# Kernel optimization log

Measured on AMD Instinct MI355X. Metric: run time of the kernel, lower is better.

Reference implementation:

```python
import jax, jax.numpy as jnp
import numpy as np

BS, C, C2, H, W = 8, 256, 128, 64, 64

def setup_inputs() -> dict:
    key = jax.random.key(0)
    ks = jax.random.split(key, 9)
    s = 0.05
    return {
        "appearance_1": jax.random.normal(ks[0], (BS, C2, H, W), jnp.float32),
        "appearance_2": jax.random.normal(ks[1], (BS, C2, H, W), jnp.float32),
        "motion": jax.random.normal(ks[2], (BS, C, H, W), jnp.float32),
        "Wq": jax.random.normal(ks[3], (C2, C2), jnp.float32) * s,
        "bq": jax.random.normal(ks[4], (C2,), jnp.float32) * s,
        "Wk": jax.random.normal(ks[5], (C2, C2), jnp.float32) * s,
        "bk": jax.random.normal(ks[6], (C2,), jnp.float32) * s,
        "Wv": jax.random.normal(ks[7], (C, C), jnp.float32) * s,
        "bv": jax.random.normal(ks[8], (C,), jnp.float32) * s,
    }

def reference(appearance_1, appearance_2, motion, Wq, bq, Wk, bk, Wv, bv):
    bs, c, h, w = motion.shape
    n = h * w
    a1 = appearance_1.reshape(bs, -1, n)   # [b, C2, N]
    a2 = appearance_2.reshape(bs, -1, n)   # [b, C2, N]
    m = motion.reshape(bs, c, n)           # [b, C,  N]
    # 1x1 convs == per-pixel linear projections
    q = jnp.einsum('oc,bcn->bon', Wq, a2) + bq[None, :, None]  # [b, C2, N]
    k = jnp.einsum('oc,bcn->bon', Wk, a1) + bk[None, :, None]  # [b, C2, N]
    v = jnp.einsum('oc,bcn->bon', Wv, m) + bv[None, :, None]   # [b, C,  N]
    # energy[b, i, j] = <q[:, i], k[:, j]> ; softmax over j
    energy = jnp.einsum('bci,bcj->bij', q, k)                  # [b, N, N]
    attention = jax.nn.softmax(energy, axis=-1)
    # out = V @ attention^T
    out = jnp.einsum('bcj,bij->bci', v, attention)             # [b, C, N]
    out = out.reshape(bs, c, h, w)
    fuse_out = out * motion
    return (fuse_out, out)
```

## Files before the change

kernel.cpp:

```cpp
#include <hip/hip_runtime.h>
#include <cstdint>
#include <cstddef>

#define BS   8
#define C    256
#define C2   128
#define NPIX 4096

typedef unsigned short u16;
typedef unsigned int   u32;
typedef __bf16 bf16_t;
typedef bf16_t bf16x8 __attribute__((ext_vector_type(8)));
typedef float  f32x16 __attribute__((ext_vector_type(16)));

__device__ __forceinline__ u16 f2bf(float f) {
    union { float ff; u32 i; } x; x.ff = f;
    u32 r = x.i + 0x7fffu + ((x.i >> 16) & 1u);
    return (u16)(r >> 16);
}

__device__ __forceinline__ void split2(float f, u16& hi, u16& lo) {
    union { float ff; u32 i; } x; x.ff = f;
    hi = (u16)(x.i >> 16);
    union { u32 i; float ff; } h; h.i = x.i & 0xffff0000u;
    union { float ff; u32 i; } r; r.ff = f - h.ff;
    lo = (u16)(r.i >> 16);
}

__device__ __forceinline__ u32 pk2(u16 a, u16 b) { return (u32)a | ((u32)b << 16); }

__global__ __launch_bounds__(256)
void prep_w(const float* __restrict__ Wq, const float* __restrict__ Wk,
            const float* __restrict__ Wv,
            u16* __restrict__ qh, u16* __restrict__ ql,
            u16* __restrict__ kh, u16* __restrict__ kl,
            u16* __restrict__ vh, u16* __restrict__ vl) {
    const int z = blockIdx.y;
    const int nelem = (z == 2) ? (C * C) : (C2 * C2);
    const int idx = (blockIdx.x * 256 + threadIdx.x) * 4;
    if (idx >= nelem) return;
    const float* src = (z == 0) ? Wq : (z == 1) ? Wk : Wv;
    u16* oh = (z == 0) ? qh : (z == 1) ? kh : vh;
    u16* ol = (z == 0) ? ql : (z == 1) ? kl : vl;
    const float4 v = *(const float4*)(src + idx);
    u16 h[4], l[4];
    split2(v.x, h[0], l[0]); split2(v.y, h[1], l[1]);
    split2(v.z, h[2], l[2]); split2(v.w, h[3], l[3]);
    *(uint2*)(oh + idx) = make_uint2(pk2(h[0], h[1]), pk2(h[2], h[3]));
    *(uint2*)(ol + idx) = make_uint2(pk2(l[0], l[1]), pk2(l[2], l[3]));
}

__global__ __launch_bounds__(256, 4)
void proj_qk(const u16* __restrict__ wh, const u16* __restrict__ wl,
             const float* __restrict__ bias,
             const float* __restrict__ x,
             u16* __restrict__ out) {
    __shared__ __align__(16) u16 Xb[2][2][2][64][8];
    const int t  = threadIdx.x;
    const int w  = t >> 6;
    const int li = t & 31;
    const int hs = (t >> 5) & 1;
    const int n0 = blockIdx.x * 64;
    const int b  = blockIdx.y;

    const int sn = t & 63;
    const int c4 = t >> 6;
    const int sh = c4 >> 1, e0 = (c4 & 1) * 4;

    const float* xbase = x + (size_t)b * C2 * NPIX + n0 + sn;

    f32x16 acc[2];
    #pragma unroll
    for (int nt = 0; nt < 2; ++nt)
        #pragma unroll
        for (int e = 0; e < 16; ++e) acc[nt][e] = 0.f;

    {
        const float* xp = xbase + (size_t)(c4 * 4) * NPIX;
        const float f0 = xp[0], f1 = xp[NPIX], f2 = xp[2 * NPIX], f3 = xp[3 * NPIX];
        u16 h[4], lo[4];
        split2(f0, h[0], lo[0]); split2(f1, h[1], lo[1]);
        split2(f2, h[2], lo[2]); split2(f3, h[3], lo[3]);
        *(uint2*)&Xb[0][0][sh][sn][e0] = make_uint2(pk2(h[0], h[1]), pk2(h[2], h[3]));
        *(uint2*)&Xb[0][1][sh][sn][e0] = make_uint2(pk2(lo[0], lo[1]), pk2(lo[2], lo[3]));
    }
    __syncthreads();

    const size_t wrow = (size_t)(w * 32 + li) * C2;
    for (int ks = 0; ks < 8; ++ks) {
        const int db = ks & 1;
        if (ks < 7) {
            const float* xp = xbase + (size_t)((ks + 1) * 16 + c4 * 4) * NPIX;
            const float f0 = xp[0], f1 = xp[NPIX], f2 = xp[2 * NPIX], f3 = xp[3 * NPIX];
            u16 h[4], lo[4];
            split2(f0, h[0], lo[0]); split2(f1, h[1], lo[1]);
            split2(f2, h[2], lo[2]); split2(f3, h[3], lo[3]);
            *(uint2*)&Xb[db ^ 1][0][sh][sn][e0] = make_uint2(pk2(h[0], h[1]), pk2(h[2], h[3]));
            *(uint2*)&Xb[db ^ 1][1][sh][sn][e0] = make_uint2(pk2(lo[0], lo[1]), pk2(lo[2], lo[3]));
        }
        const int ko = ks * 16 + hs * 8;
        const bf16x8 ah = *(const bf16x8*)(wh + wrow + ko);
        const bf16x8 al = *(const bf16x8*)(wl + wrow + ko);
        #pragma unroll
        for (int nt = 0; nt < 2; ++nt) {
            const bf16x8 bh = *(const bf16x8*)&Xb[db][0][hs][nt * 32 + li][0];
            const bf16x8 bl = *(const bf16x8*)&Xb[db][1][hs][nt * 32 + li][0];
            acc[nt] = __builtin_amdgcn_mfma_f32_32x32x16_bf16(ah, bh, acc[nt], 0, 0, 0);
            acc[nt] = __builtin_amdgcn_mfma_f32_32x32x16_bf16(ah, bl, acc[nt], 0, 0, 0);
            acc[nt] = __builtin_amdgcn_mfma_f32_32x32x16_bf16(al, bh, acc[nt], 0, 0, 0);
        }
        __syncthreads();
    }

    #pragma unroll
    for (int nt = 0; nt < 2; ++nt) {
        const int n = n0 + nt * 32 + li;
        u16* op = out + ((size_t)b * NPIX + n) * C2 + w * 32;
        #pragma unroll
        for (int g = 0; g < 4; ++g) {
            const int ob = 8 * g + 4 * hs;
            u16 p[4];
            #pragma unroll
            for (int j = 0; j < 4; ++j)
                p[j] = f2bf(acc[nt][g * 4 + j] + bias[w * 32 + ob + j]);
            *(uint2*)(op + ob) = make_uint2(pk2(p[0], p[1]), pk2(p[2], p[3]));
        }
    }
}

__global__ __launch_bounds__(256, 2)
void proj_v(const u16* __restrict__ wh, const u16* __restrict__ wl,
            const float* __restrict__ bias,
            const float* __restrict__ x,
            u16* __restrict__ out) {
    __shared__ __align__(16) u16 Xs[2][2][2][128][8];
    __shared__ __align__(16) u16 Ws[2][2][2][128][8];
    const int t  = threadIdx.x;
    const int w  = t >> 6;
    const int li = t & 31;
    const int hs = (t >> 5) & 1;
    const int n0 = blockIdx.x * 128;
    const int o0 = blockIdx.y * 128;
    const int b  = blockIdx.z;

    const int sn = t & 127;
    const int sc = t >> 7;
    const int so = t >> 1;
    const int sh2 = t & 1;

    const float* xbase = x + (size_t)b * C * NPIX + n0 + sn;
    const u16* whb = wh + (size_t)(o0 + so) * C + sh2 * 8;
    const u16* wlb = wl + (size_t)(o0 + so) * C + sh2 * 8;

    f32x16 acc[4];
    #pragma unroll
    for (int ot = 0; ot < 4; ++ot)
        #pragma unroll
        for (int e = 0; e < 16; ++e) acc[ot][e] = 0.f;

    {
        const float* xp = xbase + (size_t)(sc * 8) * NPIX;
        u16 h[8], lo[8];
        #pragma unroll
        for (int j = 0; j < 8; ++j) split2(xp[(size_t)j * NPIX], h[j], lo[j]);
        *(uint4*)&Xs[0][0][sc][sn][0] =
            make_uint4(pk2(h[0], h[1]), pk2(h[2], h[3]), pk2(h[4], h[5]), pk2(h[6], h[7]));
        *(uint4*)&Xs[0][1][sc][sn][0] =
            make_uint4(pk2(lo[0], lo[1]), pk2(lo[2], lo[3]), pk2(lo[4], lo[5]), pk2(lo[6], lo[7]));
        *(uint4*)&Ws[0][0][sh2][so][0] = *(const uint4*)(whb);
        *(uint4*)&Ws[0][1][sh2][so][0] = *(const uint4*)(wlb);
    }
    __syncthreads();

    for (int ks = 0; ks < 16; ++ks) {
        const int db = ks & 1;
        if (ks < 15) {
            const float* xp = xbase + (size_t)((ks + 1) * 16 + sc * 8) * NPIX;
            u16 h[8], lo[8];
            #pragma unroll
            for (int j = 0; j < 8; ++j) split2(xp[(size_t)j * NPIX], h[j], lo[j]);
            *(uint4*)&Xs[db ^ 1][0][sc][sn][0] =
                make_uint4(pk2(h[0], h[1]), pk2(h[2], h[3]), pk2(h[4], h[5]), pk2(h[6], h[7]));
            *(uint4*)&Xs[db ^ 1][1][sc][sn][0] =
                make_uint4(pk2(lo[0], lo[1]), pk2(lo[2], lo[3]), pk2(lo[4], lo[5]), pk2(lo[6], lo[7]));
            *(uint4*)&Ws[db ^ 1][0][sh2][so][0] = *(const uint4*)(whb + (ks + 1) * 16);
            *(uint4*)&Ws[db ^ 1][1][sh2][so][0] = *(const uint4*)(wlb + (ks + 1) * 16);
        }
        const bf16x8 xh = *(const bf16x8*)&Xs[db][0][hs][w * 32 + li][0];
        const bf16x8 xl = *(const bf16x8*)&Xs[db][1][hs][w * 32 + li][0];
        #pragma unroll
        for (int ot = 0; ot < 4; ++ot) {
            const bf16x8 bh = *(const bf16x8*)&Ws[db][0][hs][ot * 32 + li][0];
            const bf16x8 bl = *(const bf16x8*)&Ws[db][1][hs][ot * 32 + li][0];
            acc[ot] = __builtin_amdgcn_mfma_f32_32x32x16_bf16(xh, bh, acc[ot], 0, 0, 0);
            acc[ot] = __builtin_amdgcn_mfma_f32_32x32x16_bf16(xh, bl, acc[ot], 0, 0, 0);
            acc[ot] = __builtin_amdgcn_mfma_f32_32x32x16_bf16(xl, bh, acc[ot], 0, 0, 0);
        }
        __syncthreads();
    }

    #pragma unroll
    for (int ot = 0; ot < 4; ++ot) {
        const int o = o0 + ot * 32 + li;
        const float bb = bias[o];
        u16* op = out + ((size_t)b * C + o) * NPIX + n0 + w * 32;
        #pragma unroll
        for (int g = 0; g < 4; ++g) {
            u16 p[4];
            #pragma unroll
            for (int j = 0; j < 4; ++j) p[j] = f2bf(acc[ot][g * 4 + j] + bb);
            *(uint2*)(op + 8 * g + 4 * hs) = make_uint2(pk2(p[0], p[1]), pk2(p[2], p[3]));
        }
    }
}

struct SR { uint4 k[2]; uint4 v[4]; };

__device__ __forceinline__ void stg_load(const u16* __restrict__ kg,
                                         const u16* __restrict__ vg,
                                         int jt, int t, SR& R) {
    const u16* kp = kg + (size_t)jt * 32 * 128;
    #pragma unroll
    for (int q = 0; q < 2; ++q)
        R.k[q] = *(const uint4*)(kp + (size_t)(t + 256 * q) * 8);
    const u16* vp = vg + jt * 32 + (t & 3) * 8;
    #pragma unroll
    for (int q = 0; q < 4; ++q)
        R.v[q] = *(const uint4*)(vp + (size_t)((t >> 2) + 64 * q) * NPIX);
}

__device__ __forceinline__ void stg_write(u16* __restrict__ kb, u16* __restrict__ vb,
                                          int t, const SR& R) {
    #pragma unroll
    for (int q = 0; q < 2; ++q) {
        const int idx = t + 256 * q;
        const int row = idx >> 4;
        const int ch  = (idx & 15) ^ (row & 15);
        *(uint4*)(kb + row * 128 + ch * 8) = R.k[q];
    }
    #pragma unroll
    for (int q = 0; q < 4; ++q) {
        const int c   = (t >> 2) + 64 * q;
        const int rc  = c >> 1;
        const int q8  = (c & 1) * 8 + (t & 3) * 2;
        const int x   = rc & 15;
        const int ch0 = q8 ^ x;
        const int ch1 = (q8 + 1) ^ x;
        *(uint2*)(vb + rc * 64 + ch0 * 4) = make_uint2(R.v[q].x, R.v[q].y);
        *(uint2*)(vb + rc * 64 + ch1 * 4) = make_uint2(R.v[q].z, R.v[q].w);
    }
}

__global__ __launch_bounds__(256, 2)
void attn_mfma3(const u16* __restrict__ qt,
                const u16* __restrict__ kt,
                const u16* __restrict__ vn,
                float* __restrict__ opart0,
                float* __restrict__ opart1,
                float* __restrict__ sbuf) {
    __shared__ u16 Kb[2][32 * 128];
    __shared__ u16 Vb[2][128 * 64];

    const int t  = threadIdx.x;
    const int w  = t >> 6;
    const int li = t & 31;
    const int hs = (t >> 5) & 1;

    const int b  = blockIdx.x & 7;
    const int it = (blockIdx.x >> 3) & 31;
    const int h  = blockIdx.x >> 8;
    const int i0 = it * 128;
    const int iw = i0 + w * 32 + li;
    const int j0 = h * 2048;

    bf16x8 qf[8];
    {
        const u16* qp = qt + ((size_t)b * NPIX + iw) * C2 + hs * 8;
        #pragma unroll
        for (int ct = 0; ct < 8; ++ct) qf[ct] = *(const bf16x8*)(qp + ct * 16);
    }

    f32x16 oacc[8];
    #pragma unroll
    for (int ct = 0; ct < 8; ++ct)
        #pragma unroll
        for (int e = 0; e < 16; ++e) oacc[ct][e] = 0.f;

    const u16* ktb = kt + ((size_t)b * NPIX + j0) * C2;
    const u16* vnb = vn + (size_t)b * C * NPIX + j0;

    SR R;
    stg_load(ktb, vnb, 0, t, R);
    stg_write(&Kb[0][0], &Vb[0][0], t, R);
    stg_load(ktb, vnb, 1, t, R);
    __syncthreads();

    float ssl = 0.f;
    for (int itr = 0; itr < 64; ++itr) {
        const int cur = itr & 1;
        if (itr < 63) {
            stg_write(&Kb[cur ^ 1][0], &Vb[cur ^ 1][0], t, R);
            if (itr < 62) stg_load(ktb, vnb, itr + 2, t, R);
        }
        const u16* kb = &Kb[cur][0];
        const u16* vb = &Vb[cur][0];

        f32x16 s;
        #pragma unroll
        for (int e = 0; e < 16; ++e) s[e] = 0.f;
        {
            const int xr = li & 15;
            #pragma unroll
            for (int ct = 0; ct < 8; ++ct) {
                const int ch = (ct * 2 + hs) ^ xr;
                const bf16x8 kf = *(const bf16x8*)(kb + li * 128 + ch * 8);
                s = __builtin_amdgcn_mfma_f32_32x32x16_bf16(kf, qf[ct], s, 0, 0, 0);
            }
        }

        u32 pk[8];
        #pragma unroll
        for (int n = 0; n < 8; ++n) {
            const float p0 = __expf(s[2 * n]);
            const float p1 = __expf(s[2 * n + 1]);
            ssl += p0 + p1;
            pk[n] = (u32)f2bf(p0) | ((u32)f2bf(p1) << 16);
        }

        bf16x8 pf[2];
        #pragma unroll
        for (int seg = 0; seg < 2; ++seg) {
            const u32 A0 = pk[4 * seg + 0], A1 = pk[4 * seg + 1];
            const u32 A2 = pk[4 * seg + 2], A3 = pk[4 * seg + 3];
            const u32 own0 = hs ? A2 : A0, own1 = hs ? A3 : A1;
            const u32 snd0 = hs ? A0 : A2, snd1 = hs ? A1 : A3;
            const u32 rcv0 = (u32)__shfl_xor((int)snd0, 32, 64);
            const u32 rcv1 = (u32)__shfl_xor((int)snd1, 32, 64);
            union { u32 u[4]; bf16x8 v; } bb;
            bb.u[0] = hs ? rcv0 : own0;
            bb.u[1] = hs ? rcv1 : own1;
            bb.u[2] = hs ? own0 : rcv0;
            bb.u[3] = hs ? own1 : rcv1;
            pf[seg] = bb.v;
        }

        #pragma unroll
        for (int ct = 0; ct < 8; ++ct) {
            const int c  = ct * 32 + li;
            const int rc = c >> 1;
            const int x  = rc & 15;
            const u16* vr = vb + rc * 64;
            const int cb = (c & 1) * 8 + hs * 2;
            #pragma unroll
            for (int seg = 0; seg < 2; ++seg) {
                const int q8  = cb + seg * 4;
                const int ch0 = q8 ^ x;
                const int ch1 = (q8 + 1) ^ x;
                union { uint2 g[2]; bf16x8 v8; } u;
                u.g[0] = *(const uint2*)(vr + ch0 * 4);
                u.g[1] = *(const uint2*)(vr + ch1 * 4);
                oacc[ct] = __builtin_amdgcn_mfma_f32_32x32x16_bf16(u.v8, pf[seg], oacc[ct], 0, 0, 0);
            }
        }
        __syncthreads();
    }

    ssl += __shfl_xor(ssl, 32, 64);
    if (hs == 0) sbuf[((size_t)h * BS + b) * NPIX + iw] = ssl;

    float* op = h ? opart1 : opart0;
    #pragma unroll
    for (int ct = 0; ct < 8; ++ct) {
        #pragma unroll
        for (int r = 0; r < 16; ++r) {
            const int c = ct * 32 + (r & 3) + 8 * (r >> 2) + 4 * hs;
            op[((size_t)b * C + c) * NPIX + iw] = oacc[ct][r];
        }
    }
}

__global__ __launch_bounds__(256)
void attn_merge(float* __restrict__ fuse,
                float* __restrict__ outp,
                const float* __restrict__ motion,
                const float* __restrict__ sbuf) {
    const size_t idx = ((size_t)blockIdx.x * 256 + threadIdx.x) * 4;
    const int n = (int)(idx & (NPIX - 1));
    const int b = (int)(idx >> 20);
    const float4 o1 = *(const float4*)(fuse + idx);
    const float4 o2 = *(const float4*)(outp + idx);
    const float4 sa = *(const float4*)(sbuf + (size_t)b * NPIX + n);
    const float4 sb = *(const float4*)(sbuf + (size_t)(BS + b) * NPIX + n);
    float4 o;
    o.x = (o1.x + o2.x) / (sa.x + sb.x);
    o.y = (o1.y + o2.y) / (sa.y + sb.y);
    o.z = (o1.z + o2.z) / (sa.z + sb.z);
    o.w = (o1.w + o2.w) / (sa.w + sb.w);
    const float4 mv = *(const float4*)(motion + idx);
    *(float4*)(outp + idx) = o;
    *(float4*)(fuse + idx) = make_float4(o.x * mv.x, o.y * mv.y, o.z * mv.z, o.w * mv.w);
}

extern "C" void kernel_launch(void* const* d_in, const int* in_sizes, int n_in,
                              void* d_out, int out_size, void* d_ws, size_t ws_size,
                              hipStream_t stream) {
    const float* a1     = (const float*)d_in[0];
    const float* a2     = (const float*)d_in[1];
    const float* motion = (const float*)d_in[2];
    const float* Wq = (const float*)d_in[3];
    const float* bq = (const float*)d_in[4];
    const float* Wk = (const float*)d_in[5];
    const float* bk = (const float*)d_in[6];
    const float* Wv = (const float*)d_in[7];
    const float* bv = (const float*)d_in[8];

    float* outp = (float*)d_out;
    float* slot0 = outp;
    float* slot1 = outp + (size_t)BS * C * NPIX;

    u16* qws = (u16*)d_ws;
    u16* kws = qws + (size_t)BS * C2 * NPIX;
    u16* vws = kws + (size_t)BS * C2 * NPIX;
    float* sbuf = (float*)(vws + (size_t)BS * C * NPIX);
    u16* wqh = (u16*)(sbuf + (size_t)2 * BS * NPIX);
    u16* wql = wqh + C2 * C2;
    u16* wkh = wql + C2 * C2;
    u16* wkl = wkh + C2 * C2;
    u16* wvh = wkl + C2 * C2;
    u16* wvl = wvh + C * C;

    const dim3 blk(256);
    prep_w<<<dim3(64, 3), blk, 0, stream>>>(Wq, Wk, Wv, wqh, wql, wkh, wkl, wvh, wvl);
    proj_qk<<<dim3(NPIX / 64, BS), blk, 0, stream>>>(wqh, wql, bq, a2, qws);
    proj_qk<<<dim3(NPIX / 64, BS), blk, 0, stream>>>(wkh, wkl, bk, a1, kws);
    proj_v<<<dim3(NPIX / 128, 2, BS), blk, 0, stream>>>(wvh, wvl, bv, motion, vws);

    attn_mfma3<<<dim3(512), blk, 0, stream>>>(qws, kws, vws, slot0, slot1, sbuf);

    attn_merge<<<dim3((BS * C * NPIX) / 1024), blk, 0, stream>>>(
        slot0, slot1, motion, sbuf);
}
```

Measured before the change: 333.5 us.

## Merge Q/K projections into one launch and restructure projections with pre-laid-out weights

Weights are re-laid out during prep into a [c/8][o][8] fragment order so projection kernels read MFMA operands straight from global memory. The Q and K projections are merged into one launch via a z grid dimension. The V projection becomes a 64-pixel tile covering all output channels. Each block loads its whole input-channel slab into shared memory once, replacing double-buffered per-step loads and per-step barriers. The cost is larger shared memory, scalar (uncoalesced-ish) u16 output stores, and weight reads from global/L2 on every k-step.

New measurement: 329.7 us. About the same (-1.1%).

```diff
diff --git a/kernel.cpp b/kernel.cpp
--- a/kernel.cpp
+++ b/kernel.cpp
@@ -36,38 +36,72 @@
             u16* __restrict__ kh, u16* __restrict__ kl,
             u16* __restrict__ vh, u16* __restrict__ vl) {
     const int z = blockIdx.y;
-    const int nelem = (z == 2) ? (C * C) : (C2 * C2);
-    const int idx = (blockIdx.x * 256 + threadIdx.x) * 4;
-    if (idx >= nelem) return;
+    const int O = (z == 2) ? C : C2;
+    const int npair = O * O / 8;
+    const int idx = blockIdx.x * 256 + threadIdx.x;
+    if (idx >= npair) return;
+    const int o  = idx & (O - 1);
+    const int c8 = idx >> ((z == 2) ? 8 : 7);
     const float* src = (z == 0) ? Wq : (z == 1) ? Wk : Wv;
     u16* oh = (z == 0) ? qh : (z == 1) ? kh : vh;
     u16* ol = (z == 0) ? ql : (z == 1) ? kl : vl;
-    const float4 v = *(const float4*)(src + idx);
-    u16 h[4], l[4];
-    split2(v.x, h[0], l[0]); split2(v.y, h[1], l[1]);
-    split2(v.z, h[2], l[2]); split2(v.w, h[3], l[3]);
-    *(uint2*)(oh + idx) = make_uint2(pk2(h[0], h[1]), pk2(h[2], h[3]));
-    *(uint2*)(ol + idx) = make_uint2(pk2(l[0], l[1]), pk2(l[2], l[3]));
-}
-
-__global__ __launch_bounds__(256, 4)
-void proj_qk(const u16* __restrict__ wh, const u16* __restrict__ wl,
-             const float* __restrict__ bias,
-             const float* __restrict__ x,
-             u16* __restrict__ out) {
-    __shared__ __align__(16) u16 Xb[2][2][2][64][8];
+    const float4 f0 = *(const float4*)(src + (size_t)o * O + c8 * 8);
+    const float4 f1 = *(const float4*)(src + (size_t)o * O + c8 * 8 + 4);
+    u16 h[8], l[8];
+    split2(f0.x, h[0], l[0]); split2(f0.y, h[1], l[1]);
+    split2(f0.z, h[2], l[2]); split2(f0.w, h[3], l[3]);
+    split2(f1.x, h[4], l[4]); split2(f1.y, h[5], l[5]);
+    split2(f1.z, h[6], l[6]); split2(f1.w, h[7], l[7]);
+    *(uint4*)(oh + (size_t)idx * 8) =
+        make_uint4(pk2(h[0], h[1]), pk2(h[2], h[3]), pk2(h[4], h[5]), pk2(h[6], h[7]));
+    *(uint4*)(ol + (size_t)idx * 8) =
+        make_uint4(pk2(l[0], l[1]), pk2(l[2], l[3]), pk2(l[4], l[5]), pk2(l[6], l[7]));
+}
+
+__global__ __launch_bounds__(256, 2)
+void proj_qk2(const u16* __restrict__ qh2, const u16* __restrict__ ql2,
+              const float* __restrict__ bq,
+              const u16* __restrict__ kh2, const u16* __restrict__ kl2,
+              const float* __restrict__ bk,
+              const float* __restrict__ a2, const float* __restrict__ a1,
+              u16* __restrict__ qout, u16* __restrict__ kout) {
+    __shared__ __align__(16) u16 Xb[2][16][64][8];
     const int t  = threadIdx.x;
     const int w  = t >> 6;
     const int li = t & 31;
     const int hs = (t >> 5) & 1;
     const int n0 = blockIdx.x * 64;
     const int b  = blockIdx.y;
-
-    const int sn = t & 63;
-    const int c4 = t >> 6;
-    const int sh = c4 >> 1, e0 = (c4 & 1) * 4;
-
-    const float* xbase = x + (size_t)b * C2 * NPIX + n0 + sn;
+    const int z  = blockIdx.z;
+
+    const u16* wh  = z ? kh2 : qh2;
+    const u16* wl  = z ? kl2 : ql2;
+    const float* bias = z ? bk : bq;
+    const float* x = z ? a1 : a2;
+    u16* out = z ? kout : qout;
+
+    {
+        const int sn = t & 63;
+        const float* xb = x + (size_t)b * C2 * NPIX + n0 + sn;
+        float xv[4][8];
+        #pragma unroll
+        for (int q = 0; q < 4; ++q) {
+            const int c0 = (q * 4 + w) * 8;
+            #pragma unroll
+            for (int j = 0; j < 8; ++j) xv[q][j] = xb[(size_t)(c0 + j) * NPIX];
+        }
+        #pragma unroll
+        for (int q = 0; q < 4; ++q) {
+            u16 h[8], l[8];
+            #pragma unroll
+            for (int j = 0; j < 8; ++j) split2(xv[q][j], h[j], l[j]);
+            *(uint4*)&Xb[0][q * 4 + w][sn][0] =
+                make_uint4(pk2(h[0], h[1]), pk2(h[2], h[3]), pk2(h[4], h[5]), pk2(h[6], h[7]));
+            *(uint4*)&Xb[1][q * 4 + w][sn][0] =
+                make_uint4(pk2(l[0], l[1]), pk2(l[2], l[3]), pk2(l[4], l[5]), pk2(l[6], l[7]));
+        }
+    }
+    __syncthreads();
 
     f32x16 acc[2];
     #pragma unroll
@@ -75,143 +109,119 @@
         #pragma unroll
         for (int e = 0; e < 16; ++e) acc[nt][e] = 0.f;
 
-    {
-        const float* xp = xbase + (size_t)(c4 * 4) * NPIX;
-        const float f0 = xp[0], f1 = xp[NPIX], f2 = xp[2 * NPIX], f3 = xp[3 * NPIX];
-        u16 h[4], lo[4];
-        split2(f0, h[0], lo[0]); split2(f1, h[1], lo[1]);
-        split2(f2, h[2], lo[2]); split2(f3, h[3], lo[3]);
-        *(uint2*)&Xb[0][0][sh][sn][e0] = make_uint2(pk2(h[0], h[1]), pk2(h[2], h[3]));
-        *(uint2*)&Xb[0][1][sh][sn][e0] = make_uint2(pk2(lo[0], lo[1]), pk2(lo[2], lo[3]));
-    }
-    __syncthreads();
-
-    const size_t wrow = (size_t)(w * 32 + li) * C2;
+    const int ob = w * 32 + li;
+    #pragma unroll
     for (int ks = 0; ks < 8; ++ks) {
-        const int db = ks & 1;
-        if (ks < 7) {
-            const float* xp = xbase + (size_t)((ks + 1) * 16 + c4 * 4) * NPIX;
-            const float f0 = xp[0], f1 = xp[NPIX], f2 = xp[2 * NPIX], f3 = xp[3 * NPIX];
-            u16 h[4], lo[4];
-            split2(f0, h[0], lo[0]); split2(f1, h[1], lo[1]);
-            split2(f2, h[2], lo[2]); split2(f3, h[3], lo[3]);
-            *(uint2*)&Xb[db ^ 1][0][sh][sn][e0] = make_uint2(pk2(h[0], h[1]), pk2(h[2], h[3]));
-            *(uint2*)&Xb[db ^ 1][1][sh][sn][e0] = make_uint2(pk2(lo[0], lo[1]), pk2(lo[2], lo[3]));
-        }
-        const int ko = ks * 16 + hs * 8;
-        const bf16x8 ah = *(const bf16x8*)(wh + wrow + ko);
-        const bf16x8 al = *(const bf16x8*)(wl + wrow + ko);
+        const int c8 = ks * 2 + hs;
+        const bf16x8 bh = *(const bf16x8*)(wh + ((size_t)c8 * C2 + ob) * 8);
+        const bf16x8 bl = *(const bf16x8*)(wl + ((size_t)c8 * C2 + ob) * 8);
         #pragma unroll
         for (int nt = 0; nt < 2; ++nt) {
-            const bf16x8 bh = *(const bf16x8*)&Xb[db][0][hs][nt * 32 + li][0];
-            const bf16x8 bl = *(const bf16x8*)&Xb[db][1][hs][nt * 32 + li][0];
+            const bf16x8 ah = *(const bf16x8*)&Xb[0][c8][nt * 32 + li][0];
+            const bf16x8 al = *(const bf16x8*)&Xb[1][c8][nt * 32 + li][0];
             acc[nt] = __builtin_amdgcn_mfma_f32_32x32x16_bf16(ah, bh, acc[nt], 0, 0, 0);
             acc[nt] = __builtin_amdgcn_mfma_f32_32x32x16_bf16(ah, bl, acc[nt], 0, 0, 0);
             acc[nt] = __builtin_amdgcn_mfma_f32_32x32x16_bf16(al, bh, acc[nt], 0, 0, 0);
         }
-        __syncthreads();
-    }
-
-    #pragma unroll
-    for (int nt = 0; nt < 2; ++nt) {
-        const int n = n0 + nt * 32 + li;
-        u16* op = out + ((size_t)b * NPIX + n) * C2 + w * 32;
-        #pragma unroll
-        for (int g = 0; g < 4; ++g) {
-            const int ob = 8 * g + 4 * hs;
-            u16 p[4];
-            #pragma unroll
-            for (int j = 0; j < 4; ++j)
-                p[j] = f2bf(acc[nt][g * 4 + j] + bias[w * 32 + ob + j]);
-            *(uint2*)(op + ob) = make_uint2(pk2(p[0], p[1]), pk2(p[2], p[3]));
-        }
-    }
+    }
+
+    const float bb = bias[ob];
+    #pragma unroll
+    for (int nt = 0; nt < 2; ++nt)
+        #pragma unroll
+        for (int r = 0; r < 16; ++r) {
+            const int n = n0 + nt * 32 + (r & 3) + 8 * (r >> 2) + 4 * hs;
+            out[((size_t)b * NPIX + n) * C2 + ob] = f2bf(acc[nt][r] + bb);
+        }
 }
 
 __global__ __launch_bounds__(256, 2)
-void proj_v(const u16* __restrict__ wh, const u16* __restrict__ wl,
-            const float* __restrict__ bias,
-            const float* __restrict__ x,
-            u16* __restrict__ out) {
-    __shared__ __align__(16) u16 Xs[2][2][2][128][8];
-    __shared__ __align__(16) u16 Ws[2][2][2][128][8];
+void proj_v2(const u16* __restrict__ wh, const u16* __restrict__ wl,
+             const float* __restrict__ bias,
+             const float* __restrict__ x,
+             u16* __restrict__ out) {
+    __shared__ __align__(16) u16 Xb[2][32][64][8];
     const int t  = threadIdx.x;
     const int w  = t >> 6;
     const int li = t & 31;
     const int hs = (t >> 5) & 1;
-    const int n0 = blockIdx.x * 128;
-    const int o0 = blockIdx.y * 128;
-    const int b  = blockIdx.z;
-
-    const int sn = t & 127;
-    const int sc = t >> 7;
-    const int so = t >> 1;
-    const int sh2 = t & 1;
-
-    const float* xbase = x + (size_t)b * C * NPIX + n0 + sn;
-    const u16* whb = wh + (size_t)(o0 + so) * C + sh2 * 8;
-    const u16* wlb = wl + (size_t)(o0 + so) * C + sh2 * 8;
-
-    f32x16 acc[4];
-    #pragma unroll
-    for (int ot = 0; ot < 4; ++ot)
-        #pragma unroll
-        for (int e = 0; e < 16; ++e) acc[ot][e] = 0.f;
+    const int n0 = blockIdx.x * 64;
+    const int b  = blockIdx.y;
 
     {
-        const float* xp = xbase + (size_t)(sc * 8) * NPIX;
-        u16 h[8], lo[8];
-        #pragma unroll
-        for (int j = 0; j < 8; ++j) split2(xp[(size_t)j * NPIX], h[j], lo[j]);
-        *(uint4*)&Xs[0][0][sc][sn][0] =
-            make_uint4(pk2(h[0], h[1]), pk2(h[2], h[3]), pk2(h[4], h[5]), pk2(h[6], h[7]));
-        *(uint4*)&Xs[0][1][sc][sn][0] =
-            make_uint4(pk2(lo[0], lo[1]), pk2(lo[2], lo[3]), pk2(lo[4], lo[5]), pk2(lo[6], lo[7]));
-        *(uint4*)&Ws[0][0][sh2][so][0] = *(const uint4*)(whb);
-        *(uint4*)&Ws[0][1][sh2][so][0] = *(const uint4*)(wlb);
+        const int sn = t & 63;
+        const float* xb = x + (size_t)b * C * NPIX + n0 + sn;
+        #pragma unroll
+        for (int rr = 0; rr < 2; ++rr) {
+            float xv[4][8];
+            #pragma unroll
+            for (int q = 0; q < 4; ++q) {
+                const int c0 = ((rr * 4 + q) * 4 + w) * 8;
+                #pragma unroll
+                for (int j = 0; j < 8; ++j) xv[q][j] = xb[(size_t)(c0 + j) * NPIX];
+            }
+            #pragma unroll
+            for (int q = 0; q < 4; ++q) {
+                u16 h[8], l[8];
+                #pragma unroll
+                for (int j = 0; j < 8; ++j) split2(xv[q][j], h[j], l[j]);
+                const int c8 = (rr * 4 + q) * 4 + w;
+                *(uint4*)&Xb[0][c8][sn][0] =
+                    make_uint4(pk2(h[0], h[1]), pk2(h[2], h[3]), pk2(h[4], h[5]), pk2(h[6], h[7]));
+                *(uint4*)&Xb[1][c8][sn][0] =
+                    make_uint4(pk2(l[0], l[1]), pk2(l[2], l[3]), pk2(l[4], l[5]), pk2(l[6], l[7]));
+            }
+        }
     }
     __syncthreads();
 
+    f32x16 acc[2][2];
+    #pragma unroll
+    for (int ot = 0; ot < 2; ++ot)
+        #pragma unroll
+        for (int nt = 0; nt < 2; ++nt)
+            #pragma unroll
+            for (int e = 0; e < 16; ++e) acc[ot][nt][e] = 0.f;
+
+    #pragma unroll
     for (int ks = 0; ks < 16; ++ks) {
-        const int db = ks & 1;
-        if (ks < 15) {
-            const float* xp = xbase + (size_t)((ks + 1) * 16 + sc * 8) * NPIX;
-            u16 h[8], lo[8];
-            #pragma unroll
-            for (int j = 0; j < 8; ++j) split2(xp[(size_t)j * NPIX], h[j], lo[j]);
-            *(uint4*)&Xs[db ^ 1][0][sc][sn][0] =
-                make_uint4(pk2(h[0], h[1]), pk2(h[2], h[3]), pk2(h[4], h[5]), pk2(h[6], h[7]));
-            *(uint4*)&Xs[db ^ 1][1][sc][sn][0] =
-                make_uint4(pk2(lo[0], lo[1]), pk2(lo[2], lo[3]), pk2(lo[4], lo[5]), pk2(lo[6], lo[7]));
-            *(uint4*)&Ws[db ^ 1][0][sh2][so][0] = *(const uint4*)(whb + (ks + 1) * 16);
-            *(uint4*)&Ws[db ^ 1][1][sh2][so][0] = *(const uint4*)(wlb + (ks + 1) * 16);
-        }
-        const bf16x8 xh = *(const bf16x8*)&Xs[db][0][hs][w * 32 + li][0];
-        const bf16x8 xl = *(const bf16x8*)&Xs[db][1][hs][w * 32 + li][0];
-        #pragma unroll
-        for (int ot = 0; ot < 4; ++ot) {
-            const bf16x8 bh = *(const bf16x8*)&Ws[db][0][hs][ot * 32 + li][0];
-            const bf16x8 bl = *(const bf16x8*)&Ws[db][1][hs][ot * 32 + li][0];
-            acc[ot] = __builtin_amdgcn_mfma_f32_32x32x16_bf16(xh, bh, acc[ot], 0, 0, 0);
-            acc[ot] = __builtin_amdgcn_mfma_f32_32x32x16_bf16(xh, bl, acc[ot], 0, 0, 0);
-            acc[ot] = __builtin_amdgcn_mfma_f32_32x32x16_bf16(xl, bh, acc[ot], 0, 0, 0);
-        }
-        __syncthreads();
-    }
-
-    #pragma unroll
-    for (int ot = 0; ot < 4; ++ot) {
-        const int o = o0 + ot * 32 + li;
-        const float bb = bias[o];
-        u16* op = out + ((size_t)b * C + o) * NPIX + n0 + w * 32;
-        #pragma unroll
-        for (int g = 0; g < 4; ++g) {
-            u16 p[4];
-            #pragma unroll
-            for (int j = 0; j < 4; ++j) p[j] = f2bf(acc[ot][g * 4 + j] + bb);
-            *(uint2*)(op + 8 * g + 4 * hs) = make_uint2(pk2(p[0], p[1]), pk2(p[2], p[3]));
-        }
-    }
+        const int c8 = ks * 2 + hs;
+        bf16x8 ah[2], al[2], xh[2], xl[2];
+        #pragma unroll
+        for (int ot = 0; ot < 2; ++ot) {
+            const int o = w * 64 + ot * 32 + li;
+            ah[ot] = *(const bf16x8*)(wh + ((size_t)c8 * C + o) * 8);
+            al[ot] = *(const bf16x8*)(wl + ((size_t)c8 * C + o) * 8);
+        }
+        #pragma unroll
+        for (int nt = 0; nt < 2; ++nt) {
+            xh[nt] = *(const bf16x8*)&Xb[0][c8][nt * 32 + li][0];
+            xl[nt] = *(const bf16x8*)&Xb[1][c8][nt * 32 + li][0];
+        }
+        #pragma unroll
+        for (int ot = 0; ot < 2; ++ot)
+            #pragma unroll
+            for (int nt = 0; nt < 2; ++nt) {
+                acc[ot][nt] = __builtin_amdgcn_mfma_f32_32x32x16_bf16(ah[ot], xh[nt], acc[ot][nt], 0, 0, 0);
+                acc[ot][nt] = __builtin_amdgcn_mfma_f32_32x32x16_bf16(ah[ot], xl[nt], acc[ot][nt], 0, 0, 0);
+                acc[ot][nt] = __builtin_amdgcn_mfma_f32_32x32x16_bf16(al[ot], xh[nt], acc[ot][nt], 0, 0, 0);
+            }
+    }
+
+    #pragma unroll
+    for (int ot = 0; ot < 2; ++ot)
+        #pragma unroll
+        for (int nt = 0; nt < 2; ++nt)
+            #pragma unroll
+            for (int g = 0; g < 4; ++g) {
+                const int orow = w * 64 + ot * 32 + 8 * g + 4 * hs;
+                const float4 b4 = *(const float4*)&bias[orow];
+                const size_t base = ((size_t)b * C + orow) * NPIX + n0 + nt * 32 + li;
+                out[base]            = f2bf(acc[ot][nt][g * 4 + 0] + b4.x);
+                out[base + NPIX]     = f2bf(acc[ot][nt][g * 4 + 1] + b4.y);
+                out[base + 2 * NPIX] = f2bf(acc[ot][nt][g * 4 + 2] + b4.z);
+                out[base + 3 * NPIX] = f2bf(acc[ot][nt][g * 4 + 3] + b4.w);
+            }
 }
 
 struct SR { uint4 k[2]; uint4 v[4]; };
@@ -430,10 +440,10 @@
     u16* wvl = wvh + C * C;
 
     const dim3 blk(256);
-    prep_w<<<dim3(64, 3), blk, 0, stream>>>(Wq, Wk, Wv, wqh, wql, wkh, wkl, wvh, wvl);
-    proj_qk<<<dim3(NPIX / 64, BS), blk, 0, stream>>>(wqh, wql, bq, a2, qws);
-    proj_qk<<<dim3(NPIX / 64, BS), blk, 0, stream>>>(wkh, wkl, bk, a1, kws);
-    proj_v<<<dim3(NPIX / 128, 2, BS), blk, 0, stream>>>(wvh, wvl, bv, motion, vws);
+    prep_w<<<dim3(32, 3), blk, 0, stream>>>(Wq, Wk, Wv, wqh, wql, wkh, wkl, wvh, wvl);
+    proj_qk2<<<dim3(NPIX / 64, BS, 2), blk, 0, stream>>>(
+        wqh, wql, bq, wkh, wkl, bk, a2, a1, qws, kws);
+    proj_v2<<<dim3(NPIX / 64, BS), blk, 0, stream>>>(wvh, wvl, bv, motion, vws);
 
     attn_mfma3<<<dim3(512), blk, 0, stream>>>(qws, kws, vws, slot0, slot1, sbuf);
 
```
